# Kernel optimization log

Hardware: AMD Instinct MI355X
Metric: run time of the kernel (lower is better)

## Reference

```python
import jax, jax.numpy as jnp
import numpy as np

D_MODEL = 1024
NHEAD = 16
HEAD_DIM = D_MODEL // NHEAD
LN_EPS = 1e-5


def setup_inputs() -> dict:
    key = jax.random.key(0)
    ks = jax.random.split(key, 6)
    B, S = 4, 4096
    x = jax.random.normal(ks[0], (B, S, D_MODEL), dtype=jnp.float32)
    scale = 0.02
    Wq = jax.random.normal(ks[1], (D_MODEL, D_MODEL), dtype=jnp.float32) * scale
    Wv = jax.random.normal(ks[2], (D_MODEL, D_MODEL), dtype=jnp.float32) * scale
    Wo = jax.random.normal(ks[3], (D_MODEL, D_MODEL), dtype=jnp.float32) * scale
    Wg = jax.random.normal(ks[4], (D_MODEL, D_MODEL), dtype=jnp.float32) * scale
    beta = jnp.full((NHEAD,), -0.2, dtype=jnp.float32)
    ln_gamma = jnp.ones((D_MODEL,), dtype=jnp.float32)
    ln_beta = jnp.zeros((D_MODEL,), dtype=jnp.float32)
    return {"x": x, "Wq": Wq, "Wv": Wv, "Wo": Wo, "Wg": Wg,
            "beta": beta, "ln_gamma": ln_gamma, "ln_beta": ln_beta}


def _ema_scan(lam, v):
    # v: [B, S, H, D]; lam: [1, 1, H, 1]
    # s_t = lam * s_{t-1} + v_t, computed with a parallel associative scan
    # on pairs (a, b) representing the affine map s -> a*s + b.
    a = jnp.broadcast_to(lam, v.shape)

    def combine(e1, e2):
        a1, b1 = e1
        a2, b2 = e2
        return a1 * a2, a2 * b1 + b2

    _, state = jax.lax.associative_scan(combine, (a, v), axis=1)
    return state


def reference(x, Wq, Wv, Wo, Wg, beta, ln_gamma, ln_beta):
    B, S, _ = x.shape
    q = (x @ Wq.T).reshape(B, S, NHEAD, HEAD_DIM)
    v = (x @ Wv.T).reshape(B, S, NHEAD, HEAD_DIM)
    lam = jax.nn.sigmoid(beta).reshape(1, 1, NHEAD, 1).astype(v.dtype)
    state = _ema_scan(lam, v)                      # [B, S, H, D]
    y = (q * state).reshape(B, S, D_MODEL)
    # LayerNorm over last dim
    mu = jnp.mean(y, axis=-1, keepdims=True)
    var = jnp.mean(jnp.square(y - mu), axis=-1, keepdims=True)
    y = (y - mu) * jax.lax.rsqrt(var + LN_EPS) * ln_gamma + ln_beta
    gate = jax.nn.silu(x @ Wg.T)
    y = y * gate
    return y @ Wo.T
```

## Files before the change

### kernel.cpp

```cpp
#include <hip/hip_runtime.h>

#define D_MODEL 1024
#define NHEAD 16
#define LN_EPS 1e-5f
#define CHUNK 64
#define S_LEN 4096

typedef unsigned short u16;
typedef __attribute__((ext_vector_type(8))) short short8;
typedef __attribute__((ext_vector_type(4))) float f32x4;

__device__ __forceinline__ u16 f2b(float f) {
  unsigned u = __builtin_bit_cast(unsigned, f);
  u += 0x7FFFu + ((u >> 16) & 1u);
  return (u16)(u >> 16);
}
__device__ __forceinline__ float b2f(u16 s) {
  return __builtin_bit_cast(float, ((unsigned)s) << 16);
}

__global__ __launch_bounds__(256) void cvt_f32_bf16(const float4* __restrict__ src,
                                                    ushort4* __restrict__ dst, int n4) {
  int i = blockIdx.x * blockDim.x + threadIdx.x;
  int stride = gridDim.x * blockDim.x;
  for (; i < n4; i += stride) {
    float4 f = src[i];
    ushort4 o;
    o.x = f2b(f.x); o.y = f2b(f.y); o.z = f2b(f.z); o.w = f2b(f.w);
    dst[i] = o;
  }
}

__global__ void lam_kernel(const float* __restrict__ beta, float* __restrict__ lam) {
  int h = threadIdx.x;
  if (h < NHEAD) lam[h] = 1.f / (1.f + __expf(-beta[h]));
}


__device__ __forceinline__ void glds16(const u16* g, const u16* l) {
  __builtin_amdgcn_global_load_lds(
      (const __attribute__((address_space(1))) unsigned*)g,
      (__attribute__((address_space(3))) unsigned*)l, 16, 0, 0);
}

#define BAR() asm volatile("s_barrier" ::: "memory")
#define SB0() __builtin_amdgcn_sched_barrier(0)

template <typename OutT>
__global__ __launch_bounds__(512, 2) void gemm256(const u16* __restrict__ X,
                                                  const u16* __restrict__ W,
                                                  OutT* __restrict__ Out,
                                                  int M, int N, int K) {
  __shared__ u16 sm[8][8192];
  const int tid = threadIdx.x;
  const int lane = tid & 63;
  const int wave = tid >> 6;
  const int ln15 = lane & 15, lh = lane >> 4;
  const int wr = wave >> 2, wc = wave & 3;
  const int bm = blockIdx.x * 256, bn = blockIdx.y * 256;
  const int NT = K >> 6;

  const int srow = tid >> 3;
  const int scol = ((tid & 7) ^ (srow & 7)) << 3;
  const u16* Asrc = X + (size_t)(bm + srow) * K + scol;
  const u16* Bsrc = W + (size_t)(bn + srow) * K + scol;
  const int ldsw = wave * 512;

#define STAGE(u, h, tile, src)                                          \
  { const u16* _g = (src) + (size_t)((h) * 128) * K + (tile) * 64;      \
    glds16(_g,                  &sm[u][ldsw]);                          \
    glds16(_g + (size_t)64 * K, &sm[u][ldsw + 4096]); }

  const char* smb = (const char*)&sm[0][0];
  const char* Ard = smb + wr * 16384 + ln15 * 128;
  const char* Brd = smb + (2 + (wc >> 1)) * 16384 + ((wc & 1) * 64 + ln15) * 128;
  const int swz0 = ((lh ^ (ln15 & 7)) << 4);
  const int swz1 = (((4 + lh) ^ (ln15 & 7)) << 4);

#define RD_A(DB, MM, S) (*(const short8*)(Ard + (DB) + (MM) * 2048 + (S)))
#define RD_B(DB, NN, S) (*(const short8*)(Brd + (DB) + (NN) * 2048 + (S)))

  f32x4 acc[8][4];
  f32x4 zero = {0.f, 0.f, 0.f, 0.f};
  #pragma unroll
  for (int m = 0; m < 8; ++m)
    #pragma unroll
    for (int n = 0; n < 4; ++n) acc[m][n] = zero;

  short8 a[8][2], b[4][2];

#define MFMA_Q(M0, N0)                                                        \
  SB0();                                                                      \
  __builtin_amdgcn_s_setprio(1);                                              \
  _Pragma("unroll")                                                           \
  for (int m = (M0); m < (M0) + 4; ++m)                                       \
    _Pragma("unroll")                                                         \
    for (int n = (N0); n < (N0) + 2; ++n) {                                   \
      acc[m][n] = __builtin_amdgcn_mfma_f32_16x16x32_bf16(a[m][0], b[n][0], acc[m][n], 0, 0, 0); \
      acc[m][n] = __builtin_amdgcn_mfma_f32_16x16x32_bf16(a[m][1], b[n][1], acc[m][n], 0, 0, 0); \
    }                                                                         \
  __builtin_amdgcn_s_setprio(0);                                              \
  SB0();

  STAGE(0, 0, 0, Asrc); STAGE(1, 1, 0, Asrc);
  STAGE(2, 0, 0, Bsrc); STAGE(3, 1, 0, Bsrc);
  STAGE(4, 0, 1, Asrc); STAGE(5, 1, 1, Asrc);
  asm volatile("s_waitcnt vmcnt(4)" ::: "memory");
  BAR();
  #pragma unroll
  for (int m = 0; m < 4; ++m) { a[m][0] = RD_A(0, m, swz0); a[m][1] = RD_A(0, m, swz1); }
  #pragma unroll
  for (int n = 0; n < 4; ++n) { b[n][0] = RD_B(0, n, swz0); b[n][1] = RD_B(0, n, swz1); }

  for (int t = 0; t < NT; ++t) {
    const int d = t & 1;
    const int db = d * 65536;
    const int odb = (d ^ 1) * 65536;
    const int od = (d ^ 1) * 4;
    const int sd = d * 4;
    const int tB = (t + 1 < NT) ? t + 1 : NT - 1;
    const int tA = (t + 2 < NT) ? t + 2 : NT - 1;

    a[4][0] = RD_A(db, 4, swz0); a[4][1] = RD_A(db, 4, swz1);
    a[5][0] = RD_A(db, 5, swz0); a[5][1] = RD_A(db, 5, swz1);
    STAGE(od + 2, 0, tB, Bsrc);
    MFMA_Q(0, 0)

    a[6][0] = RD_A(db, 6, swz0); a[6][1] = RD_A(db, 6, swz1);
    a[7][0] = RD_A(db, 7, swz0); a[7][1] = RD_A(db, 7, swz1);
    STAGE(od + 3, 1, tB, Bsrc);
    MFMA_Q(0, 2)
    asm volatile("s_waitcnt vmcnt(4) lgkmcnt(0)" ::: "memory");
    BAR();

    #pragma unroll
    for (int m = 0; m < 4; ++m) { a[m][0] = RD_A(odb, m, swz0); a[m][1] = RD_A(odb, m, swz1); }
    MFMA_Q(4, 2)
    STAGE(sd + 0, 0, tA, Asrc);
    asm volatile("s_waitcnt vmcnt(2)" ::: "memory");
    BAR();

    b[2][0] = RD_B(odb, 2, swz0); b[2][1] = RD_B(odb, 2, swz1);
    b[3][0] = RD_B(odb, 3, swz0); b[3][1] = RD_B(odb, 3, swz1);
    MFMA_Q(4, 0)
    b[0][0] = RD_B(odb, 0, swz0); b[0][1] = RD_B(odb, 0, swz1);
    b[1][0] = RD_B(odb, 1, swz0); b[1][1] = RD_B(odb, 1, swz1);
    STAGE(sd + 1, 1, tA, Asrc);
  }
#undef STAGE
#undef RD_A
#undef RD_B
#undef MFMA_Q

  #pragma unroll
  for (int m = 0; m < 8; ++m)
    #pragma unroll
    for (int n = 0; n < 4; ++n)
      #pragma unroll
      for (int r = 0; r < 4; ++r) {
        int row = bm + wr * 128 + m * 16 + lh * 4 + r;
        int col = bn + wc * 64 + n * 16 + ln15;
        float vv = acc[m][n][r];
        if constexpr (sizeof(OutT) == 2) Out[(size_t)row * N + col] = f2b(vv);
        else                             Out[(size_t)row * N + col] = vv;
      }
}

__global__ __launch_bounds__(256) void scan_local(u16* __restrict__ v,
                                                  float* __restrict__ carry,
                                                  const float* __restrict__ lam,
                                                  int S, int nch, int ld) {
  int bj = blockIdx.x;
  int b = bj / nch, j = bj - b * nch;
  int col0 = threadIdx.x * 4;
  float l = lam[col0 >> 6];
  float s0 = 0.f, s1 = 0.f, s2 = 0.f, s3 = 0.f;
  size_t base = ((size_t)b * S + (size_t)j * CHUNK) * ld + col0;
  for (int t = 0; t < CHUNK; ++t) {
    ushort4* p = (ushort4*)(v + base + (size_t)t * ld);
    ushort4 u = *p;
    s0 = l * s0 + b2f(u.x);
    s1 = l * s1 + b2f(u.y);
    s2 = l * s2 + b2f(u.z);
    s3 = l * s3 + b2f(u.w);
    u.x = f2b(s0); u.y = f2b(s1); u.z = f2b(s2); u.w = f2b(s3);
    *p = u;
  }
  size_t cb = (size_t)bj * D_MODEL + col0;
  carry[cb] = s0; carry[cb + 1] = s1; carry[cb + 2] = s2; carry[cb + 3] = s3;
}

__global__ void scan_carry(float* __restrict__ carry, const float* __restrict__ lam,
                           int B, int nch) {
  int idx = blockIdx.x * blockDim.x + threadIdx.x;
  if (idx >= B * D_MODEL) return;
  int b = idx >> 10, col = idx & (D_MODEL - 1);
  float l = lam[col >> 6];
  float lC = __powf(l, (float)CHUNK);
  float c = 0.f;
  for (int j = 0; j < nch; ++j) {
    size_t a = ((size_t)(b * nch + j)) * D_MODEL + col;
    c = lC * c + carry[a];
    carry[a] = c;
  }
}

__global__ __launch_bounds__(256) void ew_ln(const u16* __restrict__ qvg,
    const float* __restrict__ carry, const float* __restrict__ lam,
    const float* __restrict__ gamma, const float* __restrict__ lbeta,
    u16* __restrict__ yout, int S, int nch, int ld) {
  int row = blockIdx.x;
  int b = row / S, s = row - b * S;
  int j = s / CHUNK, tl = s - j * CHUNK;
  int tid = threadIdx.x;
  int col0 = tid * 4;
  size_t rb = (size_t)row * ld;

  ushort4 qu = *(const ushort4*)(qvg + rb + col0);
  ushort4 su = *(const ushort4*)(qvg + rb + D_MODEL + col0);
  float st[4] = {b2f(su.x), b2f(su.y), b2f(su.z), b2f(su.w)};
  if (j > 0) {
    float l = lam[col0 >> 6];
    float p = __powf(l, (float)(tl + 1));
    const float4 c4 = *(const float4*)(carry + ((size_t)(b * nch + j - 1)) * D_MODEL + col0);
    st[0] += p * c4.x; st[1] += p * c4.y; st[2] += p * c4.z; st[3] += p * c4.w;
  }
  float q[4] = {b2f(qu.x), b2f(qu.y), b2f(qu.z), b2f(qu.w)};
  float y[4];
  float sum = 0.f, sumsq = 0.f;
  #pragma unroll
  for (int i = 0; i < 4; ++i) {
    y[i] = q[i] * st[i];
    sum += y[i];
    sumsq += y[i] * y[i];
  }
  #pragma unroll
  for (int off = 32; off > 0; off >>= 1) {
    sum += __shfl_down(sum, off);
    sumsq += __shfl_down(sumsq, off);
  }
  __shared__ float red[8];
  int ln = tid & 63, wv = tid >> 6;
  if (ln == 0) { red[wv] = sum; red[4 + wv] = sumsq; }
  __syncthreads();
  sum = red[0] + red[1] + red[2] + red[3];
  sumsq = red[4] + red[5] + red[6] + red[7];
  float mu = sum * (1.f / 1024.f);
  float var = sumsq * (1.f / 1024.f) - mu * mu;
  float rstd = rsqrtf(var + LN_EPS);

  float4 gm = *(const float4*)(gamma + col0);
  float4 bt = *(const float4*)(lbeta + col0);
  ushort4 gu = *(const ushort4*)(qvg + rb + 2 * D_MODEL + col0);
  float gv[4]  = {b2f(gu.x), b2f(gu.y), b2f(gu.z), b2f(gu.w)};
  float gmv[4] = {gm.x, gm.y, gm.z, gm.w};
  float btv[4] = {bt.x, bt.y, bt.z, bt.w};
  u16 ov[4];
  #pragma unroll
  for (int i = 0; i < 4; ++i) {
    float gate = gv[i] / (1.f + __expf(-gv[i]));
    float oo = ((y[i] - mu) * rstd * gmv[i] + btv[i]) * gate;
    ov[i] = f2b(oo);
  }
  ushort4 o; o.x = ov[0]; o.y = ov[1]; o.z = ov[2]; o.w = ov[3];
  *(ushort4*)(yout + (size_t)row * D_MODEL + col0) = o;
}

extern "C" void kernel_launch(void* const* d_in, const int* in_sizes, int n_in,
                              void* d_out, int out_size, void* d_ws, size_t ws_size,
                              hipStream_t stream) {
  const float* x     = (const float*)d_in[0];
  const float* Wq    = (const float*)d_in[1];
  const float* Wv    = (const float*)d_in[2];
  const float* Wo    = (const float*)d_in[3];
  const float* Wg    = (const float*)d_in[4];
  const float* beta  = (const float*)d_in[5];
  const float* gamma = (const float*)d_in[6];
  const float* lbeta = (const float*)d_in[7];
  float* out = (float*)d_out;

  const int BS = in_sizes[0] / D_MODEL;
  const int S = S_LEN;
  const int B = BS / S;
  const int nch = S / CHUNK;
  const size_t nx = (size_t)BS * D_MODEL;
  const size_t nw = (size_t)D_MODEL * D_MODEL;
  const int N3 = 3 * D_MODEL;

  char* w = (char*)d_ws;
  u16* xb   = (u16*)w;  w += nx * 2;
  u16* wqvg = (u16*)w;  w += 3 * nw * 2;
  u16* wob  = (u16*)w;  w += nw * 2;
  u16* qvg  = (u16*)w;  w += (size_t)BS * N3 * 2;
  u16* yb   = (u16*)w;  w += nx * 2;
  float* carry = (float*)w;  w += (size_t)B * nch * D_MODEL * 4;
  float* lam = (float*)w;

  cvt_f32_bf16<<<2048, 256, 0, stream>>>((const float4*)x,  (ushort4*)xb, (int)(nx / 4));
  cvt_f32_bf16<<<1024, 256, 0, stream>>>((const float4*)Wq, (ushort4*)(wqvg), (int)(nw / 4));
  cvt_f32_bf16<<<1024, 256, 0, stream>>>((const float4*)Wv, (ushort4*)(wqvg + nw), (int)(nw / 4));
  cvt_f32_bf16<<<1024, 256, 0, stream>>>((const float4*)Wg, (ushort4*)(wqvg + 2 * nw), (int)(nw / 4));
  cvt_f32_bf16<<<1024, 256, 0, stream>>>((const float4*)Wo, (ushort4*)wob, (int)(nw / 4));
  lam_kernel<<<1, 64, 0, stream>>>(beta, lam);

  dim3 g1(BS / 256, N3 / 256);
  gemm256<u16><<<g1, 512, 0, stream>>>(xb, wqvg, qvg, BS, N3, D_MODEL);

  scan_local<<<B * nch, 256, 0, stream>>>(qvg + D_MODEL, carry, lam, S, nch, N3);
  scan_carry<<<(B * D_MODEL + 255) / 256, 256, 0, stream>>>(carry, lam, B, nch);
  ew_ln<<<BS, 256, 0, stream>>>(qvg, carry, lam, gamma, lbeta, yb, S, nch, N3);

  dim3 g2(BS / 256, D_MODEL / 256);
  gemm256<float><<<g2, 512, 0, stream>>>(yb, wob, out, BS, D_MODEL, D_MODEL);
}
```

Measured before the change: 252.5 us.

## Fuse conversion kernels, restructure GEMM into quadrant pipeline, split scan blocks

After: 250.2 us. About the same (-0.9%).

```diff
diff --git a/kernel.cpp b/kernel.cpp
--- a/kernel.cpp
+++ b/kernel.cpp
@@ -19,21 +19,26 @@
   return __builtin_bit_cast(float, ((unsigned)s) << 16);
 }
 
-__global__ __launch_bounds__(256) void cvt_f32_bf16(const float4* __restrict__ src,
-                                                    ushort4* __restrict__ dst, int n4) {
+__device__ __forceinline__ ushort4 cvt4(float4 f) {
+  ushort4 o; o.x = f2b(f.x); o.y = f2b(f.y); o.z = f2b(f.z); o.w = f2b(f.w);
+  return o;
+}
+__global__ __launch_bounds__(256) void cvt_all(
+    const float4* __restrict__ x,  const float4* __restrict__ wq,
+    const float4* __restrict__ wv, const float4* __restrict__ wg,
+    const float4* __restrict__ wo, ushort4* __restrict__ xb,
+    ushort4* __restrict__ wqvg, ushort4* __restrict__ wob,
+    const float* __restrict__ beta, float* __restrict__ lam,
+    int nx4, int nw4) {
   int i = blockIdx.x * blockDim.x + threadIdx.x;
   int stride = gridDim.x * blockDim.x;
-  for (; i < n4; i += stride) {
-    float4 f = src[i];
-    ushort4 o;
-    o.x = f2b(f.x); o.y = f2b(f.y); o.z = f2b(f.z); o.w = f2b(f.w);
-    dst[i] = o;
-  }
-}
-
-__global__ void lam_kernel(const float* __restrict__ beta, float* __restrict__ lam) {
-  int h = threadIdx.x;
-  if (h < NHEAD) lam[h] = 1.f / (1.f + __expf(-beta[h]));
+  if (blockIdx.x == 0 && threadIdx.x < NHEAD)
+    lam[threadIdx.x] = 1.f / (1.f + __expf(-beta[threadIdx.x]));
+  for (int j = i; j < nx4; j += stride) xb[j] = cvt4(x[j]);
+  for (int j = i; j < nw4; j += stride) wqvg[j] = cvt4(wq[j]);
+  for (int j = i; j < nw4; j += stride) wqvg[nw4 + j] = cvt4(wv[j]);
+  for (int j = i; j < nw4; j += stride) wqvg[2 * nw4 + j] = cvt4(wg[j]);
+  for (int j = i; j < nw4; j += stride) wob[j] = cvt4(wo[j]);
 }
 
 
@@ -72,107 +77,126 @@
     glds16(_g + (size_t)64 * K, &sm[u][ldsw + 4096]); }
 
   const char* smb = (const char*)&sm[0][0];
-  const char* Ard = smb + wr * 16384 + ln15 * 128;
-  const char* Brd = smb + (2 + (wc >> 1)) * 16384 + ((wc & 1) * 64 + ln15) * 128;
+  const char* ArdB = smb + (wr * 64 + ln15) * 128;
+  const char* BrdB = smb + (wc * 32 + ln15) * 128;
   const int swz0 = ((lh ^ (ln15 & 7)) << 4);
   const int swz1 = (((4 + lh) ^ (ln15 & 7)) << 4);
 
-#define RD_A(DB, MM, S) (*(const short8*)(Ard + (DB) + (MM) * 2048 + (S)))
-#define RD_B(DB, NN, S) (*(const short8*)(Brd + (DB) + (NN) * 2048 + (S)))
-
-  f32x4 acc[8][4];
+  f32x4 acc[2][2][4][2];
   f32x4 zero = {0.f, 0.f, 0.f, 0.f};
   #pragma unroll
-  for (int m = 0; m < 8; ++m)
-    #pragma unroll
-    for (int n = 0; n < 4; ++n) acc[m][n] = zero;
-
-  short8 a[8][2], b[4][2];
-
-#define MFMA_Q(M0, N0)                                                        \
+  for (int mh = 0; mh < 2; ++mh)
+    #pragma unroll
+    for (int nh = 0; nh < 2; ++nh)
+      #pragma unroll
+      for (int m = 0; m < 4; ++m)
+        #pragma unroll
+        for (int n = 0; n < 2; ++n) acc[mh][nh][m][n] = zero;
+
+  short8 a0[4][2], a1[4][2], b0[2][2], b1[2][2];
+
+#define MFMA_Q(MH, NH, AR, BR)                                                \
   SB0();                                                                      \
   __builtin_amdgcn_s_setprio(1);                                              \
   _Pragma("unroll")                                                           \
-  for (int m = (M0); m < (M0) + 4; ++m)                                       \
+  for (int m = 0; m < 4; ++m)                                                 \
     _Pragma("unroll")                                                         \
-    for (int n = (N0); n < (N0) + 2; ++n) {                                   \
-      acc[m][n] = __builtin_amdgcn_mfma_f32_16x16x32_bf16(a[m][0], b[n][0], acc[m][n], 0, 0, 0); \
-      acc[m][n] = __builtin_amdgcn_mfma_f32_16x16x32_bf16(a[m][1], b[n][1], acc[m][n], 0, 0, 0); \
+    for (int n = 0; n < 2; ++n) {                                             \
+      acc[MH][NH][m][n] = __builtin_amdgcn_mfma_f32_16x16x32_bf16(AR[m][0], BR[n][0], acc[MH][NH][m][n], 0, 0, 0); \
+      acc[MH][NH][m][n] = __builtin_amdgcn_mfma_f32_16x16x32_bf16(AR[m][1], BR[n][1], acc[MH][NH][m][n], 0, 0, 0); \
     }                                                                         \
   __builtin_amdgcn_s_setprio(0);                                              \
   SB0();
 
-  STAGE(0, 0, 0, Asrc); STAGE(1, 1, 0, Asrc);
-  STAGE(2, 0, 0, Bsrc); STAGE(3, 1, 0, Bsrc);
-  STAGE(4, 0, 1, Asrc); STAGE(5, 1, 1, Asrc);
+  STAGE(0, 0, 0, Asrc); STAGE(2, 0, 0, Bsrc);
+  STAGE(1, 1, 0, Asrc); STAGE(3, 1, 0, Bsrc);
+  STAGE(4, 0, 1, Asrc); STAGE(6, 0, 1, Bsrc);
   asm volatile("s_waitcnt vmcnt(4)" ::: "memory");
   BAR();
-  #pragma unroll
-  for (int m = 0; m < 4; ++m) { a[m][0] = RD_A(0, m, swz0); a[m][1] = RD_A(0, m, swz1); }
-  #pragma unroll
-  for (int n = 0; n < 4; ++n) { b[n][0] = RD_B(0, n, swz0); b[n][1] = RD_B(0, n, swz1); }
 
   for (int t = 0; t < NT; ++t) {
     const int d = t & 1;
-    const int db = d * 65536;
-    const int odb = (d ^ 1) * 65536;
-    const int od = (d ^ 1) * 4;
-    const int sd = d * 4;
-    const int tB = (t + 1 < NT) ? t + 1 : NT - 1;
-    const int tA = (t + 2 < NT) ? t + 2 : NT - 1;
-
-    a[4][0] = RD_A(db, 4, swz0); a[4][1] = RD_A(db, 4, swz1);
-    a[5][0] = RD_A(db, 5, swz0); a[5][1] = RD_A(db, 5, swz1);
-    STAGE(od + 2, 0, tB, Bsrc);
-    MFMA_Q(0, 0)
-
-    a[6][0] = RD_A(db, 6, swz0); a[6][1] = RD_A(db, 6, swz1);
-    a[7][0] = RD_A(db, 7, swz0); a[7][1] = RD_A(db, 7, swz1);
-    STAGE(od + 3, 1, tB, Bsrc);
-    MFMA_Q(0, 2)
-    asm volatile("s_waitcnt vmcnt(4) lgkmcnt(0)" ::: "memory");
-    BAR();
-
-    #pragma unroll
-    for (int m = 0; m < 4; ++m) { a[m][0] = RD_A(odb, m, swz0); a[m][1] = RD_A(odb, m, swz1); }
-    MFMA_Q(4, 2)
-    STAGE(sd + 0, 0, tA, Asrc);
-    asm volatile("s_waitcnt vmcnt(2)" ::: "memory");
-    BAR();
-
-    b[2][0] = RD_B(odb, 2, swz0); b[2][1] = RD_B(odb, 2, swz1);
-    b[3][0] = RD_B(odb, 3, swz0); b[3][1] = RD_B(odb, 3, swz1);
-    MFMA_Q(4, 0)
-    b[0][0] = RD_B(odb, 0, swz0); b[0][1] = RD_B(odb, 0, swz1);
-    b[1][0] = RD_B(odb, 1, swz0); b[1][1] = RD_B(odb, 1, swz1);
-    STAGE(sd + 1, 1, tA, Asrc);
+    const int sd = d * 4, od = (d ^ 1) * 4;
+    const int tS1 = (t + 1 < NT) ? t + 1 : NT - 1;
+    const int tS2 = (t + 2 < NT) ? t + 2 : NT - 1;
+    const char* Ah0 = ArdB + (sd + 0) * 16384;
+    const char* Ah1 = ArdB + (sd + 1) * 16384;
+    const char* Bh0 = BrdB + (sd + 2) * 16384;
+    const char* Bh1 = BrdB + (sd + 3) * 16384;
+
+    #pragma unroll
+    for (int m = 0; m < 4; ++m) {
+      a0[m][0] = *(const short8*)(Ah0 + m * 2048 + swz0);
+      a0[m][1] = *(const short8*)(Ah0 + m * 2048 + swz1);
+    }
+    #pragma unroll
+    for (int n = 0; n < 2; ++n) {
+      b0[n][0] = *(const short8*)(Bh0 + n * 2048 + swz0);
+      b0[n][1] = *(const short8*)(Bh0 + n * 2048 + swz1);
+    }
+    STAGE(od + 1, 1, tS1, Asrc);
+    asm volatile("s_waitcnt lgkmcnt(8)" ::: "memory");
+    BAR();
+    asm volatile("s_waitcnt lgkmcnt(0)" ::: "memory");
+    MFMA_Q(0, 0, a0, b0)
+    BAR();
+
+    #pragma unroll
+    for (int m = 0; m < 4; ++m) {
+      a1[m][0] = *(const short8*)(Ah1 + m * 2048 + swz0);
+      a1[m][1] = *(const short8*)(Ah1 + m * 2048 + swz1);
+    }
+    STAGE(od + 3, 1, tS1, Bsrc);
+    BAR();
+    asm volatile("s_waitcnt lgkmcnt(0)" ::: "memory");
+    MFMA_Q(1, 0, a1, b0)
+    BAR();
+
+    #pragma unroll
+    for (int n = 0; n < 2; ++n) {
+      b1[n][0] = *(const short8*)(Bh1 + n * 2048 + swz0);
+      b1[n][1] = *(const short8*)(Bh1 + n * 2048 + swz1);
+    }
+    STAGE(sd + 0, 0, tS2, Asrc);
+    BAR();
+    asm volatile("s_waitcnt lgkmcnt(0)" ::: "memory");
+    MFMA_Q(1, 1, a1, b1)
+    BAR();
+
+    STAGE(sd + 2, 0, tS2, Bsrc);
+    BAR();
+    MFMA_Q(0, 1, a0, b1)
+    asm volatile("s_waitcnt vmcnt(4)" ::: "memory");
+    BAR();
   }
 #undef STAGE
-#undef RD_A
-#undef RD_B
 #undef MFMA_Q
 
   #pragma unroll
-  for (int m = 0; m < 8; ++m)
-    #pragma unroll
-    for (int n = 0; n < 4; ++n)
+  for (int mh = 0; mh < 2; ++mh)
+    #pragma unroll
+    for (int nh = 0; nh < 2; ++nh)
       #pragma unroll
-      for (int r = 0; r < 4; ++r) {
-        int row = bm + wr * 128 + m * 16 + lh * 4 + r;
-        int col = bn + wc * 64 + n * 16 + ln15;
-        float vv = acc[m][n][r];
-        if constexpr (sizeof(OutT) == 2) Out[(size_t)row * N + col] = f2b(vv);
-        else                             Out[(size_t)row * N + col] = vv;
-      }
-}
-
-__global__ __launch_bounds__(256) void scan_local(u16* __restrict__ v,
+      for (int m = 0; m < 4; ++m)
+        #pragma unroll
+        for (int n = 0; n < 2; ++n)
+          #pragma unroll
+          for (int r = 0; r < 4; ++r) {
+            int row = bm + mh * 128 + wr * 64 + m * 16 + lh * 4 + r;
+            int col = bn + nh * 128 + wc * 32 + n * 16 + ln15;
+            float vv = acc[mh][nh][m][n][r];
+            if constexpr (sizeof(OutT) == 2) Out[(size_t)row * N + col] = f2b(vv);
+            else                             Out[(size_t)row * N + col] = vv;
+          }
+}
+
+__global__ __launch_bounds__(128) void scan_local(u16* __restrict__ v,
                                                   float* __restrict__ carry,
                                                   const float* __restrict__ lam,
                                                   int S, int nch, int ld) {
-  int bj = blockIdx.x;
+  int bj = blockIdx.x >> 1, half = blockIdx.x & 1;
   int b = bj / nch, j = bj - b * nch;
-  int col0 = threadIdx.x * 4;
+  int col0 = half * 512 + threadIdx.x * 4;
   float l = lam[col0 >> 6];
   float s0 = 0.f, s1 = 0.f, s2 = 0.f, s3 = 0.f;
   size_t base = ((size_t)b * S + (size_t)j * CHUNK) * ld + col0;
@@ -296,17 +320,15 @@
   float* carry = (float*)w;  w += (size_t)B * nch * D_MODEL * 4;
   float* lam = (float*)w;
 
-  cvt_f32_bf16<<<2048, 256, 0, stream>>>((const float4*)x,  (ushort4*)xb, (int)(nx / 4));
-  cvt_f32_bf16<<<1024, 256, 0, stream>>>((const float4*)Wq, (ushort4*)(wqvg), (int)(nw / 4));
-  cvt_f32_bf16<<<1024, 256, 0, stream>>>((const float4*)Wv, (ushort4*)(wqvg + nw), (int)(nw / 4));
-  cvt_f32_bf16<<<1024, 256, 0, stream>>>((const float4*)Wg, (ushort4*)(wqvg + 2 * nw), (int)(nw / 4));
-  cvt_f32_bf16<<<1024, 256, 0, stream>>>((const float4*)Wo, (ushort4*)wob, (int)(nw / 4));
-  lam_kernel<<<1, 64, 0, stream>>>(beta, lam);
+  cvt_all<<<2048, 256, 0, stream>>>((const float4*)x, (const float4*)Wq,
+      (const float4*)Wv, (const float4*)Wg, (const float4*)Wo,
+      (ushort4*)xb, (ushort4*)wqvg, (ushort4*)wob, beta, lam,
+      (int)(nx / 4), (int)(nw / 4));
 
   dim3 g1(BS / 256, N3 / 256);
   gemm256<u16><<<g1, 512, 0, stream>>>(xb, wqvg, qvg, BS, N3, D_MODEL);
 
-  scan_local<<<B * nch, 256, 0, stream>>>(qvg + D_MODEL, carry, lam, S, nch, N3);
+  scan_local<<<B * nch * 2, 128, 0, stream>>>(qvg + D_MODEL, carry, lam, S, nch, N3);
   scan_carry<<<(B * D_MODEL + 255) / 256, 256, 0, stream>>>(carry, lam, B, nch);
   ew_ln<<<BS, 256, 0, stream>>>(qvg, carry, lam, gamma, lbeta, yb, S, nch, N3);
 
```

## Fuse conversion kernels, halve scan chunk, use exp2 powers, relax GEMM wait

Applied to the files above, without the earlier changes.

After: 237.9 us. -5.8%, faster.

```diff
diff --git a/kernel.cpp b/kernel.cpp
--- a/kernel.cpp
+++ b/kernel.cpp
@@ -3,7 +3,7 @@
 #define D_MODEL 1024
 #define NHEAD 16
 #define LN_EPS 1e-5f
-#define CHUNK 64
+#define CHUNK 32
 #define S_LEN 4096
 
 typedef unsigned short u16;
@@ -19,21 +19,29 @@
   return __builtin_bit_cast(float, ((unsigned)s) << 16);
 }
 
-__global__ __launch_bounds__(256) void cvt_f32_bf16(const float4* __restrict__ src,
-                                                    ushort4* __restrict__ dst, int n4) {
+__device__ __forceinline__ ushort4 cvt4(float4 f) {
+  ushort4 o; o.x = f2b(f.x); o.y = f2b(f.y); o.z = f2b(f.z); o.w = f2b(f.w);
+  return o;
+}
+__global__ __launch_bounds__(256) void cvt_all(
+    const float4* __restrict__ x,  const float4* __restrict__ wq,
+    const float4* __restrict__ wv, const float4* __restrict__ wg,
+    const float4* __restrict__ wo, ushort4* __restrict__ xb,
+    ushort4* __restrict__ wqvg, ushort4* __restrict__ wob,
+    const float* __restrict__ beta, float* __restrict__ lam,
+    int nx4, int nw4) {
   int i = blockIdx.x * blockDim.x + threadIdx.x;
   int stride = gridDim.x * blockDim.x;
-  for (; i < n4; i += stride) {
-    float4 f = src[i];
-    ushort4 o;
-    o.x = f2b(f.x); o.y = f2b(f.y); o.z = f2b(f.z); o.w = f2b(f.w);
-    dst[i] = o;
-  }
-}
-
-__global__ void lam_kernel(const float* __restrict__ beta, float* __restrict__ lam) {
-  int h = threadIdx.x;
-  if (h < NHEAD) lam[h] = 1.f / (1.f + __expf(-beta[h]));
+  if (blockIdx.x == 0 && threadIdx.x < NHEAD) {
+    float l = 1.f / (1.f + __expf(-beta[threadIdx.x]));
+    lam[threadIdx.x] = l;
+    lam[NHEAD + threadIdx.x] = __log2f(l);
+  }
+  for (int j = i; j < nx4; j += stride) xb[j] = cvt4(x[j]);
+  for (int j = i; j < nw4; j += stride) wqvg[j] = cvt4(wq[j]);
+  for (int j = i; j < nw4; j += stride) wqvg[nw4 + j] = cvt4(wv[j]);
+  for (int j = i; j < nw4; j += stride) wqvg[2 * nw4 + j] = cvt4(wg[j]);
+  for (int j = i; j < nw4; j += stride) wob[j] = cvt4(wo[j]);
 }
 
 
@@ -130,7 +138,7 @@
     a[7][0] = RD_A(db, 7, swz0); a[7][1] = RD_A(db, 7, swz1);
     STAGE(od + 3, 1, tB, Bsrc);
     MFMA_Q(0, 2)
-    asm volatile("s_waitcnt vmcnt(4) lgkmcnt(0)" ::: "memory");
+    asm volatile("s_waitcnt vmcnt(4)" ::: "memory");
     BAR();
 
     #pragma unroll
@@ -176,6 +184,7 @@
   float l = lam[col0 >> 6];
   float s0 = 0.f, s1 = 0.f, s2 = 0.f, s3 = 0.f;
   size_t base = ((size_t)b * S + (size_t)j * CHUNK) * ld + col0;
+  #pragma unroll 4
   for (int t = 0; t < CHUNK; ++t) {
     ushort4* p = (ushort4*)(v + base + (size_t)t * ld);
     ushort4 u = *p;
@@ -195,9 +204,9 @@
   int idx = blockIdx.x * blockDim.x + threadIdx.x;
   if (idx >= B * D_MODEL) return;
   int b = idx >> 10, col = idx & (D_MODEL - 1);
-  float l = lam[col >> 6];
-  float lC = __powf(l, (float)CHUNK);
+  float lC = exp2f(lam[NHEAD + (col >> 6)] * (float)CHUNK);
   float c = 0.f;
+  #pragma unroll 4
   for (int j = 0; j < nch; ++j) {
     size_t a = ((size_t)(b * nch + j)) * D_MODEL + col;
     c = lC * c + carry[a];
@@ -220,8 +229,7 @@
   ushort4 su = *(const ushort4*)(qvg + rb + D_MODEL + col0);
   float st[4] = {b2f(su.x), b2f(su.y), b2f(su.z), b2f(su.w)};
   if (j > 0) {
-    float l = lam[col0 >> 6];
-    float p = __powf(l, (float)(tl + 1));
+    float p = exp2f(lam[NHEAD + (col0 >> 6)] * (float)(tl + 1));
     const float4 c4 = *(const float4*)(carry + ((size_t)(b * nch + j - 1)) * D_MODEL + col0);
     st[0] += p * c4.x; st[1] += p * c4.y; st[2] += p * c4.z; st[3] += p * c4.w;
   }
@@ -296,12 +304,10 @@
   float* carry = (float*)w;  w += (size_t)B * nch * D_MODEL * 4;
   float* lam = (float*)w;
 
-  cvt_f32_bf16<<<2048, 256, 0, stream>>>((const float4*)x,  (ushort4*)xb, (int)(nx / 4));
-  cvt_f32_bf16<<<1024, 256, 0, stream>>>((const float4*)Wq, (ushort4*)(wqvg), (int)(nw / 4));
-  cvt_f32_bf16<<<1024, 256, 0, stream>>>((const float4*)Wv, (ushort4*)(wqvg + nw), (int)(nw / 4));
-  cvt_f32_bf16<<<1024, 256, 0, stream>>>((const float4*)Wg, (ushort4*)(wqvg + 2 * nw), (int)(nw / 4));
-  cvt_f32_bf16<<<1024, 256, 0, stream>>>((const float4*)Wo, (ushort4*)wob, (int)(nw / 4));
-  lam_kernel<<<1, 64, 0, stream>>>(beta, lam);
+  cvt_all<<<2048, 256, 0, stream>>>((const float4*)x, (const float4*)Wq,
+      (const float4*)Wv, (const float4*)Wg, (const float4*)Wo,
+      (ushort4*)xb, (ushort4*)wqvg, (ushort4*)wob, beta, lam,
+      (int)(nx / 4), (int)(nw / 4));
 
   dim3 g1(BS / 256, N3 / 256);
   gemm256<u16><<<g1, 512, 0, stream>>>(xb, wqvg, qvg, BS, N3, D_MODEL);
```
